# Kernel tuning notes

Measured on AMD Instinct MI355X. Metric: run time of the kernel, lower is better.

The kernel has to match this reference:

```python
import jax, jax.numpy as jnp
import numpy as np

ALPHA = 0.1  # LeakyReLU slope

def _leaky(v):
    return jnp.where(v >= 0, v, ALPHA * v)

def setup_inputs() -> dict:
    key = jax.random.key(0)
    k1, k2, k3 = jax.random.split(key, 3)
    B, D_IN, D1, D2 = 262144, 200, 150, 100
    x = jax.random.normal(k1, (B, D_IN), dtype=jnp.float32)
    W1 = jax.random.normal(k2, (D_IN, D1), dtype=jnp.float32) * 0.05
    b1 = jnp.zeros((D1,), dtype=jnp.float32)
    W2 = jax.random.normal(k3, (D1, D2), dtype=jnp.float32) * 0.05
    b2 = jnp.zeros((D2,), dtype=jnp.float32)
    return {"x": x, "W1": W1, "b1": b1, "W2": W2, "b2": b2}

def reference(x, W1, b1, W2, b2):
    # Original loops per sample: dense(200->150)+LeakyReLU, mean -> out1;
    # dense(150->100)+LeakyReLU, mean -> out2. Batched here as single GEMMs.
    h1 = _leaky(x @ W1 + b1)           # [B, 150]
    out1 = jnp.mean(h1, axis=-1)       # [B]
    h2 = _leaky(h1 @ W2 + b2)          # [B, 100]
    out2 = jnp.mean(h2, axis=-1)       # [B]
    return (out1, out2)
```

## Files before the change

kernel.cpp:

```cpp
#include <hip/hip_runtime.h>

typedef unsigned short u16;
typedef unsigned int u32;
typedef __bf16 bf16x8 __attribute__((ext_vector_type(8)));
typedef float f32x4 __attribute__((ext_vector_type(4)));

#define W2F_OFF 71680
#define B1_OFF 107520
#define B2_OFF 108160
#define WS_BYTES 108608

__device__ __align__(256) unsigned char g_wbuf[WS_BYTES];

__device__ __forceinline__ u16 f2bf(float f) {
  __bf16 b = (__bf16)f;
  return __builtin_bit_cast(u16, b);
}
__device__ __forceinline__ u32 pk2bf(float a, float b) {
  return (u32)f2bf(a) | ((u32)f2bf(b) << 16);
}

__global__ void prep_kernel(const float* __restrict__ W1, const float* __restrict__ b1,
                            const float* __restrict__ W2, const float* __restrict__ b2)
{
  const int stride = gridDim.x * blockDim.x;
  const int tid0 = blockIdx.x * blockDim.x + threadIdx.x;
  u16* w1f = (u16*)g_wbuf;
  for (int e = tid0; e < 35840; e += stride) {
    int j = e & 7, l = (e >> 3) & 63, nt = (e >> 9) % 10, kt = e / 5120;
    int k = kt * 32 + ((l >> 4) << 3) + j;
    int n = nt * 16 + (l & 15);
    w1f[e] = (k < 200 && n < 150) ? f2bf(W1[k * 150 + n]) : (u16)0;
  }
  u16* w2f = (u16*)(g_wbuf + W2F_OFF);
  for (int e = tid0; e < 17920; e += stride) {
    int j = e & 7, l = (e >> 3) & 63, nt = (e >> 9) % 7, kt = e / 3584;
    int k = kt * 32 + ((l >> 4) << 3) + j;
    int n = nt * 16 + (l & 15);
    w2f[e] = (k < 150 && n < 100) ? f2bf(W2[k * 100 + n]) : (u16)0;
  }
  float* b1p = (float*)(g_wbuf + B1_OFF);
  for (int e = tid0; e < 160; e += stride) b1p[e] = (e < 150) ? b1[e] : 0.f;
  float* b2p = (float*)(g_wbuf + B2_OFF);
  for (int e = tid0; e < 112; e += stride) b2p[e] = (e < 100) ? b2[e] : 0.f;
}

__global__ __launch_bounds__(256, 4)
void fused_mlp(const float* __restrict__ x, float* __restrict__ out, int B)
{
  __shared__ __align__(16) u16 xs[12800];
  __shared__ float ps[2][2][64];

  const int tid = threadIdx.x;
  const int lane = tid & 63;
  const int wv = tid >> 6;
  const int h = wv & 1;
  const int pr = wv >> 1;
  const int cl = lane & 15, gr = lane >> 4;
  const long r0 = (long)blockIdx.x * 64;

  const u16* w1g = (const u16*)g_wbuf;
  const u16* w2g = (const u16*)(g_wbuf + W2F_OFF);

  const float* xg = x + r0 * 200;
  #pragma unroll
  for (int i = 0; i < 13; ++i) {
    int c = tid + i * 256;
    if (c < 3200) {
      int row = c / 50, kc = c % 50;
      float4 v = *reinterpret_cast<const float4*>(xg + row * 200 + kc * 4);
      int k0 = kc * 4;
      int mt = row >> 4;
      int idx;
      if (k0 < 192) {
        int F = mt * 6 + (k0 >> 5);
        int fl = (row & 15) | (((k0 & 31) >> 3) << 4);
        int slot = fl ^ (F & 7);
        idx = (F * 64 + slot) * 8 + (k0 & 7);
      } else {
        idx = 12288 + mt * 128 + (row & 15) * 8 + (k0 - 192);
      }
      uint2 p;
      p.x = pk2bf(v.x, v.y);
      p.y = pk2bf(v.z, v.w);
      *reinterpret_cast<uint2*>(&xs[idx]) = p;
    }
  }

  bf16x8 bfr[5];
  #pragma unroll
  for (int nt = 0; nt < 5; ++nt)
    bfr[nt] = *reinterpret_cast<const bf16x8*>(w1g + ((0 * 10 + 5 * h + nt) * 64 + lane) * 8);

  __syncthreads();

  const int mt0 = pr * 2, mt1 = pr * 2 + 1;
  const f32x4 zz = {0.f, 0.f, 0.f, 0.f};
  f32x4 acc1[2][5];
  #pragma unroll
  for (int i = 0; i < 2; ++i)
    #pragma unroll
    for (int nt = 0; nt < 5; ++nt) acc1[i][nt] = zz;

  #pragma unroll
  for (int kt = 0; kt < 7; ++kt) {
    bf16x8 bnx[5];
    if (kt < 6) {
      #pragma unroll
      for (int nt = 0; nt < 5; ++nt)
        bnx[nt] = *reinterpret_cast<const bf16x8*>(w1g + (((kt + 1) * 10 + 5 * h + nt) * 64 + lane) * 8);
    }
    bf16x8 a0, a1;
    if (kt < 6) {
      int F0 = mt0 * 6 + kt, F1 = mt1 * 6 + kt;
      a0 = *reinterpret_cast<const bf16x8*>(&xs[(F0 * 64 + (lane ^ (F0 & 7))) * 8]);
      a1 = *reinterpret_cast<const bf16x8*>(&xs[(F1 * 64 + (lane ^ (F1 & 7))) * 8]);
    } else {
      union { bf16x8 v; u32 w[4]; } A0, A1;
      A0.v = *reinterpret_cast<const bf16x8*>(&xs[12288 + mt0 * 128 + cl * 8]);
      A1.v = *reinterpret_cast<const bf16x8*>(&xs[12288 + mt1 * 128 + cl * 8]);
      if (gr != 0) {
        A0.w[0] = A0.w[1] = A0.w[2] = A0.w[3] = 0u;
        A1.w[0] = A1.w[1] = A1.w[2] = A1.w[3] = 0u;
      }
      a0 = A0.v; a1 = A1.v;
    }
    #pragma unroll
    for (int nt = 0; nt < 5; ++nt) {
      acc1[0][nt] = __builtin_amdgcn_mfma_f32_16x16x32_bf16(a0, bfr[nt], acc1[0][nt], 0, 0, 0);
      acc1[1][nt] = __builtin_amdgcn_mfma_f32_16x16x32_bf16(a1, bfr[nt], acc1[1][nt], 0, 0, 0);
    }
    if (kt < 6) {
      #pragma unroll
      for (int nt = 0; nt < 5; ++nt) bfr[nt] = bnx[nt];
    }
  }
  __syncthreads();

  const float* b1p = (const float*)(g_wbuf + B1_OFF);
  float b1v[5];
  #pragma unroll
  for (int nt = 0; nt < 5; ++nt) b1v[nt] = b1p[(5 * h + nt) * 16 + cl];

  float rs0[4] = {0, 0, 0, 0}, rs1[4] = {0, 0, 0, 0};
  #pragma unroll
  for (int nt = 0; nt < 5; ++nt) {
    int k2 = (5 * h + nt) * 16 + cl;
    int kt2 = k2 >> 5;
    int l2base = 16 * ((k2 & 31) >> 3);
    int e2 = k2 & 7;
    #pragma unroll
    for (int j = 0; j < 4; ++j) {
      int l2 = gr * 4 + j + l2base;
      float hv = acc1[0][nt][j] + b1v[nt];
      hv = (hv >= 0.f) ? hv : 0.1f * hv;
      rs0[j] += hv;
      xs[((mt0 * 5 + kt2) * 64 + l2) * 8 + e2] = f2bf(hv);
      float gv = acc1[1][nt][j] + b1v[nt];
      gv = (gv >= 0.f) ? gv : 0.1f * gv;
      rs1[j] += gv;
      xs[((mt1 * 5 + kt2) * 64 + l2) * 8 + e2] = f2bf(gv);
    }
  }
  #pragma unroll
  for (int j = 0; j < 4; ++j) {
    float s0 = rs0[j], s1 = rs1[j];
    #pragma unroll
    for (int mask = 1; mask < 16; mask <<= 1) {
      s0 += __shfl_xor(s0, mask, 64);
      s1 += __shfl_xor(s1, mask, 64);
    }
    if (cl == 0) {
      ps[0][h][mt0 * 16 + gr * 4 + j] = s0;
      ps[0][h][mt1 * 16 + gr * 4 + j] = s1;
    }
  }
  __syncthreads();

  if (wv == 0)
    out[r0 + lane] = (ps[0][0][lane] + ps[0][1][lane]) * (1.f / 150.f);

  f32x4 acc2[2][4];
  #pragma unroll
  for (int i = 0; i < 2; ++i)
    #pragma unroll
    for (int nt = 0; nt < 4; ++nt) acc2[i][nt] = zz;

  bf16x8 b2r[4];
  #pragma unroll
  for (int nt = 0; nt < 4; ++nt)
    if (nt < 3 || h == 0)
      b2r[nt] = *reinterpret_cast<const bf16x8*>(w2g + ((0 * 7 + 4 * h + nt) * 64 + lane) * 8);

  #pragma unroll
  for (int kt = 0; kt < 5; ++kt) {
    bf16x8 bnx[4];
    if (kt < 4) {
      #pragma unroll
      for (int nt = 0; nt < 4; ++nt)
        if (nt < 3 || h == 0)
          bnx[nt] = *reinterpret_cast<const bf16x8*>(w2g + (((kt + 1) * 7 + 4 * h + nt) * 64 + lane) * 8);
    }
    bf16x8 a0 = *reinterpret_cast<const bf16x8*>(&xs[((mt0 * 5 + kt) * 64 + lane) * 8]);
    bf16x8 a1 = *reinterpret_cast<const bf16x8*>(&xs[((mt1 * 5 + kt) * 64 + lane) * 8]);
    #pragma unroll
    for (int nt = 0; nt < 4; ++nt) {
      if (nt < 3 || h == 0) {
        acc2[0][nt] = __builtin_amdgcn_mfma_f32_16x16x32_bf16(a0, b2r[nt], acc2[0][nt], 0, 0, 0);
        acc2[1][nt] = __builtin_amdgcn_mfma_f32_16x16x32_bf16(a1, b2r[nt], acc2[1][nt], 0, 0, 0);
      }
    }
    if (kt < 4) {
      #pragma unroll
      for (int nt = 0; nt < 4; ++nt)
        if (nt < 3 || h == 0) b2r[nt] = bnx[nt];
    }
  }

  const float* b2p = (const float*)(g_wbuf + B2_OFF);
  float b2v[4];
  #pragma unroll
  for (int nt = 0; nt < 4; ++nt)
    b2v[nt] = (nt < 3 || h == 0) ? b2p[(4 * h + nt) * 16 + cl] : 0.f;

  float t0[4] = {0, 0, 0, 0}, t1[4] = {0, 0, 0, 0};
  #pragma unroll
  for (int nt = 0; nt < 4; ++nt) {
    if (nt < 3 || h == 0) {
      #pragma unroll
      for (int j = 0; j < 4; ++j) {
        float hv = acc2[0][nt][j] + b2v[nt];
        hv = (hv >= 0.f) ? hv : 0.1f * hv;
        t0[j] += hv;
        float gv = acc2[1][nt][j] + b2v[nt];
        gv = (gv >= 0.f) ? gv : 0.1f * gv;
        t1[j] += gv;
      }
    }
  }
  #pragma unroll
  for (int j = 0; j < 4; ++j) {
    float s0 = t0[j], s1 = t1[j];
    #pragma unroll
    for (int mask = 1; mask < 16; mask <<= 1) {
      s0 += __shfl_xor(s0, mask, 64);
      s1 += __shfl_xor(s1, mask, 64);
    }
    if (cl == 0) {
      ps[1][h][mt0 * 16 + gr * 4 + j] = s0;
      ps[1][h][mt1 * 16 + gr * 4 + j] = s1;
    }
  }
  __syncthreads();

  if (wv == 0)
    out[B + r0 + lane] = (ps[1][0][lane] + ps[1][1][lane]) * (1.f / 100.f);
}

extern "C" void kernel_launch(void* const* d_in, const int* in_sizes, int n_in,
                              void* d_out, int out_size, void* d_ws, size_t ws_size,
                              hipStream_t stream)
{
  const float* x  = (const float*)d_in[0];
  const float* W1 = (const float*)d_in[1];
  const float* b1 = (const float*)d_in[2];
  const float* W2 = (const float*)d_in[3];
  const float* b2 = (const float*)d_in[4];
  float* out = (float*)d_out;
  const int B = in_sizes[0] / 200;

  prep_kernel<<<64, 256, 0, stream>>>(W1, b1, W2, b2);
  fused_mlp<<<B / 64, 256, 0, stream>>>(x, out, B);
}
```

Before: 71.49 us.

## Load x directly into MFMA fragments from global, dropping LDS staging

Each wave now reads its input rows from global memory straight into registers in the MFMA A-operand layout. It converts them to bf16 in registers and prefetches the next K-slice while the current one computes. This removes the LDS write/read round-trip for x and one block-wide barrier, and shrinks the shared buffer to hold only the hidden activations per wave pair. In exchange, both column-half waves load the same x rows, which doubles L1/L2 request traffic, and each lane's accesses are less coalesced than the old block-wide float4 sweep.

```diff
diff --git a/kernel.cpp b/kernel.cpp
--- a/kernel.cpp
+++ b/kernel.cpp
@@ -48,7 +48,7 @@
 __global__ __launch_bounds__(256, 4)
 void fused_mlp(const float* __restrict__ x, float* __restrict__ out, int B)
 {
-  __shared__ __align__(16) u16 xs[12800];
+  __shared__ __align__(16) u16 hbuf[2][5120];
   __shared__ float ps[2][2][64];
 
   const int tid = threadIdx.x;
@@ -58,43 +58,23 @@
   const int pr = wv >> 1;
   const int cl = lane & 15, gr = lane >> 4;
   const long r0 = (long)blockIdx.x * 64;
+  const long wr0 = r0 + pr * 32;
 
   const u16* w1g = (const u16*)g_wbuf;
   const u16* w2g = (const u16*)(g_wbuf + W2F_OFF);
 
-  const float* xg = x + r0 * 200;
-  #pragma unroll
-  for (int i = 0; i < 13; ++i) {
-    int c = tid + i * 256;
-    if (c < 3200) {
-      int row = c / 50, kc = c % 50;
-      float4 v = *reinterpret_cast<const float4*>(xg + row * 200 + kc * 4);
-      int k0 = kc * 4;
-      int mt = row >> 4;
-      int idx;
-      if (k0 < 192) {
-        int F = mt * 6 + (k0 >> 5);
-        int fl = (row & 15) | (((k0 & 31) >> 3) << 4);
-        int slot = fl ^ (F & 7);
-        idx = (F * 64 + slot) * 8 + (k0 & 7);
-      } else {
-        idx = 12288 + mt * 128 + (row & 15) * 8 + (k0 - 192);
-      }
-      uint2 p;
-      p.x = pk2bf(v.x, v.y);
-      p.y = pk2bf(v.z, v.w);
-      *reinterpret_cast<uint2*>(&xs[idx]) = p;
-    }
-  }
-
+  const float* xb0 = x + (wr0 + cl) * 200 + gr * 8;
+  const float* xb1 = xb0 + 16 * 200;
+
+  float4 cA0 = *reinterpret_cast<const float4*>(xb0);
+  float4 cA1 = *reinterpret_cast<const float4*>(xb0 + 4);
+  float4 cA2 = *reinterpret_cast<const float4*>(xb1);
+  float4 cA3 = *reinterpret_cast<const float4*>(xb1 + 4);
   bf16x8 bfr[5];
   #pragma unroll
   for (int nt = 0; nt < 5; ++nt)
     bfr[nt] = *reinterpret_cast<const bf16x8*>(w1g + ((0 * 10 + 5 * h + nt) * 64 + lane) * 8);
 
-  __syncthreads();
-
-  const int mt0 = pr * 2, mt1 = pr * 2 + 1;
   const f32x4 zz = {0.f, 0.f, 0.f, 0.f};
   f32x4 acc1[2][5];
   #pragma unroll
@@ -104,38 +84,38 @@
 
   #pragma unroll
   for (int kt = 0; kt < 7; ++kt) {
+    float4 nA0, nA1, nA2, nA3;
     bf16x8 bnx[5];
     if (kt < 6) {
+      const int ko = (kt + 1) * 32;
+      if (kt + 1 < 6 || gr == 0) {
+        nA0 = *reinterpret_cast<const float4*>(xb0 + ko);
+        nA1 = *reinterpret_cast<const float4*>(xb0 + ko + 4);
+        nA2 = *reinterpret_cast<const float4*>(xb1 + ko);
+        nA3 = *reinterpret_cast<const float4*>(xb1 + ko + 4);
+      } else {
+        nA0 = nA1 = nA2 = nA3 = make_float4(0.f, 0.f, 0.f, 0.f);
+      }
       #pragma unroll
       for (int nt = 0; nt < 5; ++nt)
         bnx[nt] = *reinterpret_cast<const bf16x8*>(w1g + (((kt + 1) * 10 + 5 * h + nt) * 64 + lane) * 8);
     }
-    bf16x8 a0, a1;
+    union { bf16x8 v; u32 w[4]; } A0, A1;
+    A0.w[0] = pk2bf(cA0.x, cA0.y); A0.w[1] = pk2bf(cA0.z, cA0.w);
+    A0.w[2] = pk2bf(cA1.x, cA1.y); A0.w[3] = pk2bf(cA1.z, cA1.w);
+    A1.w[0] = pk2bf(cA2.x, cA2.y); A1.w[1] = pk2bf(cA2.z, cA2.w);
+    A1.w[2] = pk2bf(cA3.x, cA3.y); A1.w[3] = pk2bf(cA3.z, cA3.w);
+    #pragma unroll
+    for (int nt = 0; nt < 5; ++nt) {
+      acc1[0][nt] = __builtin_amdgcn_mfma_f32_16x16x32_bf16(A0.v, bfr[nt], acc1[0][nt], 0, 0, 0);
+      acc1[1][nt] = __builtin_amdgcn_mfma_f32_16x16x32_bf16(A1.v, bfr[nt], acc1[1][nt], 0, 0, 0);
+    }
     if (kt < 6) {
-      int F0 = mt0 * 6 + kt, F1 = mt1 * 6 + kt;
-      a0 = *reinterpret_cast<const bf16x8*>(&xs[(F0 * 64 + (lane ^ (F0 & 7))) * 8]);
-      a1 = *reinterpret_cast<const bf16x8*>(&xs[(F1 * 64 + (lane ^ (F1 & 7))) * 8]);
-    } else {
-      union { bf16x8 v; u32 w[4]; } A0, A1;
-      A0.v = *reinterpret_cast<const bf16x8*>(&xs[12288 + mt0 * 128 + cl * 8]);
-      A1.v = *reinterpret_cast<const bf16x8*>(&xs[12288 + mt1 * 128 + cl * 8]);
-      if (gr != 0) {
-        A0.w[0] = A0.w[1] = A0.w[2] = A0.w[3] = 0u;
-        A1.w[0] = A1.w[1] = A1.w[2] = A1.w[3] = 0u;
-      }
-      a0 = A0.v; a1 = A1.v;
-    }
-    #pragma unroll
-    for (int nt = 0; nt < 5; ++nt) {
-      acc1[0][nt] = __builtin_amdgcn_mfma_f32_16x16x32_bf16(a0, bfr[nt], acc1[0][nt], 0, 0, 0);
-      acc1[1][nt] = __builtin_amdgcn_mfma_f32_16x16x32_bf16(a1, bfr[nt], acc1[1][nt], 0, 0, 0);
-    }
-    if (kt < 6) {
+      cA0 = nA0; cA1 = nA1; cA2 = nA2; cA3 = nA3;
       #pragma unroll
       for (int nt = 0; nt < 5; ++nt) bfr[nt] = bnx[nt];
     }
   }
-  __syncthreads();
 
   const float* b1p = (const float*)(g_wbuf + B1_OFF);
   float b1v[5];
@@ -155,11 +135,11 @@
       float hv = acc1[0][nt][j] + b1v[nt];
       hv = (hv >= 0.f) ? hv : 0.1f * hv;
       rs0[j] += hv;
-      xs[((mt0 * 5 + kt2) * 64 + l2) * 8 + e2] = f2bf(hv);
+      hbuf[pr][(kt2 * 64 + l2) * 8 + e2] = f2bf(hv);
       float gv = acc1[1][nt][j] + b1v[nt];
       gv = (gv >= 0.f) ? gv : 0.1f * gv;
       rs1[j] += gv;
-      xs[((mt1 * 5 + kt2) * 64 + l2) * 8 + e2] = f2bf(gv);
+      hbuf[pr][((5 + kt2) * 64 + l2) * 8 + e2] = f2bf(gv);
     }
   }
   #pragma unroll
@@ -171,14 +151,14 @@
       s1 += __shfl_xor(s1, mask, 64);
     }
     if (cl == 0) {
-      ps[0][h][mt0 * 16 + gr * 4 + j] = s0;
-      ps[0][h][mt1 * 16 + gr * 4 + j] = s1;
+      ps[0][h][pr * 32 + gr * 4 + j]      = s0;
+      ps[0][h][pr * 32 + 16 + gr * 4 + j] = s1;
     }
   }
   __syncthreads();
 
-  if (wv == 0)
-    out[r0 + lane] = (ps[0][0][lane] + ps[0][1][lane]) * (1.f / 150.f);
+  if (tid < 64)
+    out[r0 + tid] = (ps[0][0][tid] + ps[0][1][tid]) * (1.f / 150.f);
 
   f32x4 acc2[2][4];
   #pragma unroll
@@ -194,15 +174,15 @@
 
   #pragma unroll
   for (int kt = 0; kt < 5; ++kt) {
-    bf16x8 bnx[4];
+    bf16x8 bnx2[4];
     if (kt < 4) {
       #pragma unroll
       for (int nt = 0; nt < 4; ++nt)
         if (nt < 3 || h == 0)
-          bnx[nt] = *reinterpret_cast<const bf16x8*>(w2g + (((kt + 1) * 7 + 4 * h + nt) * 64 + lane) * 8);
-    }
-    bf16x8 a0 = *reinterpret_cast<const bf16x8*>(&xs[((mt0 * 5 + kt) * 64 + lane) * 8]);
-    bf16x8 a1 = *reinterpret_cast<const bf16x8*>(&xs[((mt1 * 5 + kt) * 64 + lane) * 8]);
+          bnx2[nt] = *reinterpret_cast<const bf16x8*>(w2g + (((kt + 1) * 7 + 4 * h + nt) * 64 + lane) * 8);
+    }
+    bf16x8 a0 = *reinterpret_cast<const bf16x8*>(&hbuf[pr][(kt * 64 + lane) * 8]);
+    bf16x8 a1 = *reinterpret_cast<const bf16x8*>(&hbuf[pr][((5 + kt) * 64 + lane) * 8]);
     #pragma unroll
     for (int nt = 0; nt < 4; ++nt) {
       if (nt < 3 || h == 0) {
@@ -213,7 +193,7 @@
     if (kt < 4) {
       #pragma unroll
       for (int nt = 0; nt < 4; ++nt)
-        if (nt < 3 || h == 0) b2r[nt] = bnx[nt];
+        if (nt < 3 || h == 0) b2r[nt] = bnx2[nt];
     }
   }
 
@@ -247,14 +227,14 @@
       s1 += __shfl_xor(s1, mask, 64);
     }
     if (cl == 0) {
-      ps[1][h][mt0 * 16 + gr * 4 + j] = s0;
-      ps[1][h][mt1 * 16 + gr * 4 + j] = s1;
+      ps[1][h][pr * 32 + gr * 4 + j]      = s0;
+      ps[1][h][pr * 32 + 16 + gr * 4 + j] = s1;
     }
   }
   __syncthreads();
 
-  if (wv == 0)
-    out[B + r0 + lane] = (ps[1][0][lane] + ps[1][1][lane]) * (1.f / 100.f);
+  if (tid < 64)
+    out[B + r0 + tid] = (ps[1][0][tid] + ps[1][1][tid]) * (1.f / 100.f);
 }
 
 extern "C" void kernel_launch(void* const* d_in, const int* in_sizes, int n_in,
```

Measured after the change: 77.97 us. +9.1%, slower.
